# Optimization experiments

Hardware: AMD Instinct MI355X
Metric: run time of the kernel (lower is better)

The kernel has to match this reference:

```python
import jax, jax.numpy as jnp
import numpy as np

SEQ, WORD, EMBED, NHEAD = 2048, 1024, 128, 16


def setup_inputs() -> dict:
    key = jax.random.key(0)
    ks = jax.random.split(key, 6)
    sw = 1.0 / np.sqrt(WORD)  # xavier-ish scale for linear weights
    sp = 1.0 / np.sqrt(EMBED * NHEAD)
    return {
        "x": jax.random.normal(ks[0], (SEQ, WORD), jnp.float32),
        "Wq": jax.random.normal(ks[1], (NHEAD, WORD, EMBED), jnp.float32) * sw,
        "bq": jnp.zeros((NHEAD, EMBED), jnp.float32),
        "Wk": jax.random.normal(ks[2], (NHEAD, WORD, EMBED), jnp.float32) * sw,
        "bk": jnp.zeros((NHEAD, EMBED), jnp.float32),
        "Wv": jax.random.normal(ks[3], (NHEAD, WORD, EMBED), jnp.float32) * sw,
        "bv": jnp.zeros((NHEAD, EMBED), jnp.float32),
        "proj": jax.random.normal(ks[4], (NHEAD * EMBED, EMBED), jnp.float32) * sp,
    }


def reference(x, Wq, bq, Wk, bk, Wv, bv, proj):
    # Batched-head equivalent of the per-head Attention ModuleList loop.
    # x: [S, W]; Wq/Wk/Wv: [H, W, E]; b*: [H, E]; proj: [H*E, E]
    Q = jnp.einsum("sw,hwe->hse", x, Wq) + bq[:, None, :]
    K = jnp.einsum("sw,hwe->hse", x, Wk) + bk[:, None, :]
    V = jnp.einsum("sw,hwe->hse", x, Wv) + bv[:, None, :]
    scale = 1.0 / jnp.sqrt(jnp.asarray(EMBED, x.dtype))
    scores = jnp.einsum("hqe,hke->hqk", Q, K) * scale  # [H, S, S]
    attn = jax.nn.softmax(scores, axis=-1)
    Z = jnp.einsum("hqk,hke->hqe", attn, V)  # [H, S, E]
    # torch.cat([...], dim=1): per-head outputs side-by-side -> [S, H*E]
    Z_s = jnp.transpose(Z, (1, 0, 2)).reshape(x.shape[0], -1)
    return Z_s @ proj  # [S, E]
```

## Files before the change

kernel.cpp:

```cpp
#include <hip/hip_runtime.h>
#include <stdint.h>

#define GAS __attribute__((address_space(1)))
#define LAS __attribute__((address_space(3)))

typedef unsigned short u16;
typedef __attribute__((ext_vector_type(8))) __bf16 bf16x8;
typedef __attribute__((ext_vector_type(4))) float f32x4;
typedef __attribute__((ext_vector_type(4))) unsigned short u16x4;

#define SEQ 2048
#define WORD 1024
#define EMBED 128
#define NHEAD 16

__device__ __forceinline__ u16 f2b(float f) {
  return __builtin_bit_cast(u16, (__bf16)f);
}

__device__ __forceinline__ long qfrag_off(int qrow, int e) {
  return ((((long)(qrow >> 4)) * 4 + (e >> 5)) * 64 + ((e >> 3) & 3) * 16 +
          (qrow & 15)) * 8 + (e & 7);
}

__global__ __launch_bounds__(256) void cast_x_kernel(const float* __restrict__ x,
                                                     u16* __restrict__ xb) {
  int i = (blockIdx.x * 256 + threadIdx.x) * 4;
  float4 v = *(const float4*)(x + i);
  ushort4 o;
  o.x = f2b(v.x); o.y = f2b(v.y); o.z = f2b(v.z); o.w = f2b(v.w);
  *(ushort4*)(xb + i) = o;
}

__global__ __launch_bounds__(256) void transpose_cast_kernel(
    const float* __restrict__ s0, const float* __restrict__ s1,
    const float* __restrict__ s2, u16* __restrict__ d0, u16* __restrict__ d1,
    u16* __restrict__ d2, int R, int C, long stride, int zsel) {
  __shared__ float tile[32][33];
  const float* s;
  u16* d;
  if (zsel) {
    int z = blockIdx.z;
    int wsel = z >> 4, hh = z & 15;
    s = (wsel == 0 ? s0 : wsel == 1 ? s1 : s2) + (long)hh * stride;
    d = (wsel == 0 ? d0 : wsel == 1 ? d1 : d2) + (long)hh * stride;
  } else {
    s = s0; d = d0;
  }
  int r0 = blockIdx.x * 32, c0 = blockIdx.y * 32;
  int tx = threadIdx.x & 31, ty = threadIdx.x >> 5;
#pragma unroll
  for (int i = 0; i < 4; ++i)
    tile[ty + i * 8][tx] = s[(long)(r0 + ty + i * 8) * C + c0 + tx];
  __syncthreads();
#pragma unroll
  for (int i = 0; i < 4; ++i)
    d[(long)(c0 + ty + i * 8) * R + r0 + tx] = f2b(tile[tx][ty + i * 8]);
}

template <int MODE>
__device__ __forceinline__ void gemm128(const u16* __restrict__ A, const u16* __restrict__ B,
                                        void* __restrict__ Cp, int lda, int ldb, int ldc,
                                        int ksteps, const float* biasN, const float* biasM,
                                        float scale, int rowbase) {
  __shared__ u16 lA[128 * 64];
  __shared__ u16 lB[128 * 64];
  const int tid = threadIdx.x;
  const int l = tid & 63, w = tid >> 6;
  const int quad = l >> 4, ln = l & 15;
  const int wm = w >> 1, wn = w & 1;
  f32x4 acc[4][4] = {};
  for (int ks = 0; ks < ksteps; ++ks) {
    const u16* Ak = A + ks * 64;
    const u16* Bk = B + ks * 64;
    __syncthreads();
#pragma unroll
    for (int i = 0; i < 4; ++i) {
      int idx = w * 256 + i * 64 + l;
      int r = idx >> 3, cp = idx & 7;
      int cg = cp ^ (r & 7);
      __builtin_amdgcn_global_load_lds((const GAS void*)(Ak + (long)r * lda + cg * 8),
                                       (LAS void*)(lA + (w * 256 + i * 64) * 8), 16, 0, 0);
      __builtin_amdgcn_global_load_lds((const GAS void*)(Bk + (long)r * ldb + cg * 8),
                                       (LAS void*)(lB + (w * 256 + i * 64) * 8), 16, 0, 0);
    }
    __syncthreads();
    bf16x8 af[2][4], bfv[2][4];
#pragma unroll
    for (int kc = 0; kc < 2; ++kc) {
#pragma unroll
      for (int i = 0; i < 4; ++i) {
        int c = kc * 4 + quad;
        int rm = wm * 64 + i * 16 + ln;
        af[kc][i] = *(const bf16x8*)(lA + rm * 64 + ((c ^ (rm & 7)) * 8));
        int rn = wn * 64 + i * 16 + ln;
        bfv[kc][i] = *(const bf16x8*)(lB + rn * 64 + ((c ^ (rn & 7)) * 8));
      }
    }
#pragma unroll
    for (int kc = 0; kc < 2; ++kc)
#pragma unroll
      for (int i = 0; i < 4; ++i)
#pragma unroll
        for (int j = 0; j < 4; ++j)
          acc[i][j] = __builtin_amdgcn_mfma_f32_16x16x32_bf16(af[kc][i], bfv[kc][j],
                                                              acc[i][j], 0, 0, 0);
  }
#pragma unroll
  for (int i = 0; i < 4; ++i) {
#pragma unroll
    for (int j = 0; j < 4; ++j) {
      int row0 = wm * 64 + i * 16 + quad * 4;
      int col = wn * 64 + j * 16 + ln;
      float bn = biasN ? biasN[col] : 0.f;
#pragma unroll
      for (int reg = 0; reg < 4; ++reg) {
        int row = row0 + reg;
        float bm = biasM ? biasM[row] : 0.f;
        float v = (acc[i][j][reg] + bn + bm) * scale;
        if constexpr (MODE == 0) {
          ((float*)Cp)[(long)row * ldc + col] = v;
        } else if constexpr (MODE == 1) {
          ((u16*)Cp)[(long)row * ldc + col] = f2b(v);
        } else {
          ((u16*)Cp)[qfrag_off(rowbase + row, col)] = f2b(v);
        }
      }
    }
  }
}

__global__ __launch_bounds__(256, 3) void qkv_gemm_kernel(
    const u16* __restrict__ xb, const u16* __restrict__ Wqt, const u16* __restrict__ Wkt,
    const u16* __restrict__ Wvt, const float* __restrict__ bq, const float* __restrict__ bk,
    const float* __restrict__ bv, u16* __restrict__ Qf, u16* __restrict__ Km,
    u16* __restrict__ Vt) {
  const int t = blockIdx.x;
  const int h = blockIdx.y;
  const int which = blockIdx.z;
  const float qscale = 0.12753042123789493f;
  if (which == 0) {
    gemm128<2>(xb + t * 128 * WORD, Wqt + h * EMBED * WORD,
               Qf + (long)h * 262144, WORD, WORD, 0,
               WORD / 64, bq + h * EMBED, nullptr, qscale, t * 128);
  } else if (which == 1) {
    gemm128<1>(xb + t * 128 * WORD, Wkt + h * EMBED * WORD,
               Km + (long)h * SEQ * EMBED + t * 128 * EMBED, WORD, WORD, EMBED,
               WORD / 64, bk + h * EMBED, nullptr, 1.f, 0);
  } else {
    gemm128<1>(Wvt + h * EMBED * WORD, xb + t * 128 * WORD,
               Vt + (long)h * EMBED * SEQ + t * 128, WORD, WORD, SEQ,
               WORD / 64, nullptr, bv + h * EMBED, 1.f, 0);
  }
}

__global__ __launch_bounds__(256, 2) void attn_kernel(const u16* __restrict__ Qf,
                                                      const u16* __restrict__ Km,
                                                      const u16* __restrict__ Vt,
                                                      u16* __restrict__ Zs) {
  __shared__ u16 lKV[2][2][8192];
  __shared__ u16 lP[4][32 * 40];
  const int h = blockIdx.y, qb = blockIdx.x;
  const int tid = threadIdx.x;
  const int l = tid & 63, w = tid >> 6, quad = l >> 4, ln = l & 15;
  const int wr = w >> 1, wk = w & 1;
  const u16* Kh = Km + (long)h * SEQ * EMBED;
  const u16* Vh = Vt + (long)h * EMBED * SEQ;
  const u16* Qfh = Qf + (long)h * 262144;
  u16* Pw = lP[w];

  bf16x8 qf[2][4];
#pragma unroll
  for (int rs = 0; rs < 2; ++rs)
#pragma unroll
    for (int kc = 0; kc < 4; ++kc)
      qf[rs][kc] = *(const bf16x8*)(Qfh + (((qb * 4 + wr * 2 + rs) * 4 + kc) * 64 + l) * 8);

  const __bf16 ov = (ln == 0) ? (__bf16)1.0f : (__bf16)0.0f;
  const bf16x8 onesf = {ov, ov, ov, ov, ov, ov, ov, ov};

  f32x4 oacc[2][8] = {};
  f32x4 lacc[2] = {};

  auto stage = [&](int sup, int buf) {
#pragma unroll
    for (int j = 0; j < 4; ++j) {
      int ck = j * 256 + w * 64 + l;
      int kr = ck >> 4, cg = (ck & 15) ^ (kr & 15);
      __builtin_amdgcn_global_load_lds(
          (const GAS void*)(Kh + (sup * 64 + kr) * EMBED + cg * 8),
          (LAS void*)(&lKV[buf][0][(j * 256 + w * 64) * 8]), 16, 0, 0);
      int cv = j * 256 + w * 64 + l;
      int rv = cv >> 3, cgv = (cv & 7) ^ (rv & 7);
      __builtin_amdgcn_global_load_lds(
          (const GAS void*)(Vh + (long)rv * SEQ + sup * 64 + cgv * 8),
          (LAS void*)(&lKV[buf][1][(j * 256 + w * 64) * 8]), 16, 0, 0);
    }
  };

  stage(0, 0);
  for (int sup = 0; sup < SEQ / 64; ++sup) {
    const int cur = sup & 1;
    __syncthreads();
    if (sup + 1 < SEQ / 64) stage(sup + 1, cur ^ 1);
    const u16* Kb = lKV[cur][0];
    const u16* Vb = lKV[cur][1];
#pragma unroll
    for (int ns = 0; ns < 2; ++ns) {
      f32x4 sacc[2] = {};
#pragma unroll
      for (int kc = 0; kc < 4; ++kc) {
        int ks = wk * 32 + ns * 16 + ln;
        bf16x8 kf = *(const bf16x8*)(Kb + ks * 128 + (((kc * 4 + quad) ^ (ks & 15)) * 8));
#pragma unroll
        for (int rs = 0; rs < 2; ++rs)
          sacc[rs] = __builtin_amdgcn_mfma_f32_16x16x32_bf16(kf, qf[rs][kc],
                                                             sacc[rs], 0, 0, 0);
      }
#pragma unroll
      for (int rs = 0; rs < 2; ++rs) {
        u16x4 pk;
        pk.x = f2b(exp2f(sacc[rs][0]));
        pk.y = f2b(exp2f(sacc[rs][1]));
        pk.z = f2b(exp2f(sacc[rs][2]));
        pk.w = f2b(exp2f(sacc[rs][3]));
        *(u16x4*)(Pw + (rs * 16 + ln) * 40 + (ns * 4 + quad) * 4) = pk;
      }
    }
    bf16x8 pa[2];
#pragma unroll
    for (int rs = 0; rs < 2; ++rs)
      pa[rs] = *(const bf16x8*)(Pw + (rs * 16 + ln) * 40 + quad * 8);
    bf16x8 vf[8];
#pragma unroll
    for (int es = 0; es < 8; ++es) {
      int er = es * 16 + ln;
      vf[es] = *(const bf16x8*)(Vb + er * 64 + (((wk * 4 + quad) ^ (er & 7)) * 8));
    }
#pragma unroll
    for (int es = 0; es < 8; ++es)
#pragma unroll
      for (int rs = 0; rs < 2; ++rs)
        oacc[rs][es] = __builtin_amdgcn_mfma_f32_16x16x32_bf16(pa[rs], vf[es],
                                                               oacc[rs][es], 0, 0, 0);
#pragma unroll
    for (int rs = 0; rs < 2; ++rs)
      lacc[rs] = __builtin_amdgcn_mfma_f32_16x16x32_bf16(pa[rs], onesf, lacc[rs], 0, 0, 0);
  }
  __syncthreads();
  float* lO = (float*)lKV;
  float* lL = lO + 64 * 132;
  if (wk == 1) {
#pragma unroll
    for (int rs = 0; rs < 2; ++rs) {
#pragma unroll
      for (int es = 0; es < 8; ++es)
#pragma unroll
        for (int r = 0; r < 4; ++r)
          lO[(wr * 32 + rs * 16 + quad * 4 + r) * 132 + es * 16 + ln] = oacc[rs][es][r];
      if (ln == 0)
#pragma unroll
        for (int r = 0; r < 4; ++r)
          lL[wr * 32 + rs * 16 + quad * 4 + r] = lacc[rs][r];
    }
  }
  __syncthreads();
  if (wk == 0) {
#pragma unroll
    for (int rs = 0; rs < 2; ++rs)
#pragma unroll
      for (int r = 0; r < 4; ++r) {
        int grow = wr * 32 + rs * 16 + quad * 4 + r;
        float lsum = __shfl(lacc[rs][r], l & 48) + lL[grow];
        float rl = 1.f / lsum;
        int srow = qb * 64 + grow;
#pragma unroll
        for (int es = 0; es < 8; ++es) {
          float o = oacc[rs][es][r] + lO[grow * 132 + es * 16 + ln];
          Zs[(long)srow * (NHEAD * EMBED) + h * EMBED + es * 16 + ln] = f2b(o * rl);
        }
      }
  }
}

__global__ __launch_bounds__(256, 2) void final_gemm_kernel(const u16* __restrict__ Zs,
                                                            const u16* __restrict__ projT,
                                                            float* __restrict__ pbuf) {
  const int t = blockIdx.x;
  const int kc = blockIdx.y;
  gemm128<0>(Zs + (long)t * 128 * (NHEAD * EMBED) + kc * 256, projT + kc * 256,
             pbuf + (long)kc * SEQ * EMBED + t * 128 * EMBED,
             NHEAD * EMBED, NHEAD * EMBED, EMBED, 4, nullptr, nullptr, 1.f, 0);
}

__global__ __launch_bounds__(256) void reduce_kernel(const float* __restrict__ pbuf,
                                                     float* __restrict__ out) {
  int i = (blockIdx.x * 256 + threadIdx.x) * 4;
  float4 s = {0.f, 0.f, 0.f, 0.f};
#pragma unroll
  for (int kc = 0; kc < 8; ++kc) {
    float4 v = *(const float4*)(pbuf + (long)kc * SEQ * EMBED + i);
    s.x += v.x; s.y += v.y; s.z += v.z; s.w += v.w;
  }
  *(float4*)(out + i) = s;
}

extern "C" void kernel_launch(void* const* d_in, const int* in_sizes, int n_in,
                              void* d_out, int out_size, void* d_ws, size_t ws_size,
                              hipStream_t stream) {
  const float* x    = (const float*)d_in[0];
  const float* Wq   = (const float*)d_in[1];
  const float* bq   = (const float*)d_in[2];
  const float* Wk   = (const float*)d_in[3];
  const float* bk   = (const float*)d_in[4];
  const float* Wv   = (const float*)d_in[5];
  const float* bv   = (const float*)d_in[6];
  const float* proj = (const float*)d_in[7];
  float* out = (float*)d_out;

  char* ws = (char*)d_ws;
  u16* xb    = (u16*)(ws);
  u16* Wqt   = (u16*)(ws + (4L << 20));
  u16* Wkt   = (u16*)(ws + (8L << 20));
  u16* Wvt   = (u16*)(ws + (12L << 20));
  u16* projT = (u16*)(ws + (16L << 20));
  u16* Qf    = (u16*)(ws + (17L << 20));
  u16* Km    = (u16*)(ws + (26L << 20));
  u16* Vt    = (u16*)(ws + (35L << 20));
  u16* Zs    = (u16*)(ws + (44L << 20));
  float* pbuf = (float*)(ws);

  cast_x_kernel<<<dim3(SEQ * WORD / 1024), dim3(256), 0, stream>>>(x, xb);
  transpose_cast_kernel<<<dim3(WORD / 32, EMBED / 32, 48), dim3(256), 0, stream>>>(
      Wq, Wk, Wv, Wqt, Wkt, Wvt, WORD, EMBED, (long)WORD * EMBED, 1);
  transpose_cast_kernel<<<dim3(SEQ / 32, EMBED / 32, 1), dim3(256), 0, stream>>>(
      proj, nullptr, nullptr, projT, nullptr, nullptr, SEQ, EMBED, 0, 0);

  qkv_gemm_kernel<<<dim3(16, NHEAD, 3), dim3(256), 0, stream>>>(
      xb, Wqt, Wkt, Wvt, bq, bk, bv, Qf, Km, Vt);

  attn_kernel<<<dim3(32, NHEAD), dim3(256), 0, stream>>>(Qf, Km, Vt, Zs);

  final_gemm_kernel<<<dim3(16, 8), dim3(256), 0, stream>>>(Zs, projT, pbuf);
  reduce_kernel<<<dim3(SEQ * EMBED / 1024), dim3(256), 0, stream>>>(pbuf, out);
}
```

Measured before the change: 208.1 us.

## Store K and V in MFMA fragment layout and load directly to registers

The QKV GEMM now writes K and V in pre-swizzled MFMA fragment order, the same way Q already was. The attention kernel then loads K/V fragments straight from global memory into registers with software prefetch, instead of staging them through double-buffered LDS with barriers. It also linearises the grid so that consecutive blocks share a query block across heads. This removes the LDS staging and the per-iteration __syncthreads. The cost is that each wave re-reads K/V from global/L2 without sharing them through LDS, and register pressure rises.

```diff
diff --git a/kernel.cpp b/kernel.cpp
--- a/kernel.cpp
+++ b/kernel.cpp
@@ -18,9 +18,13 @@
   return __builtin_bit_cast(u16, (__bf16)f);
 }
 
-__device__ __forceinline__ long qfrag_off(int qrow, int e) {
-  return ((((long)(qrow >> 4)) * 4 + (e >> 5)) * 64 + ((e >> 3) & 3) * 16 +
-          (qrow & 15)) * 8 + (e & 7);
+__device__ __forceinline__ long qfrag_off(int row, int e) {
+  return ((((long)(row >> 4)) * 4 + (e >> 5)) * 64 + ((e >> 3) & 3) * 16 +
+          (row & 15)) * 8 + (e & 7);
+}
+__device__ __forceinline__ long vfrag_off(int er, int key) {
+  return (((((long)(key >> 5)) * 8) + (er >> 4)) * 64 +
+          ((key >> 3) & 3) * 16 + (er & 15)) * 8 + (key & 7);
 }
 
 __global__ __launch_bounds__(256) void cast_x_kernel(const float* __restrict__ x,
@@ -62,7 +66,7 @@
 __device__ __forceinline__ void gemm128(const u16* __restrict__ A, const u16* __restrict__ B,
                                         void* __restrict__ Cp, int lda, int ldb, int ldc,
                                         int ksteps, const float* biasN, const float* biasM,
-                                        float scale, int rowbase) {
+                                        float scale, int rowbase, int colbase) {
   __shared__ u16 lA[128 * 64];
   __shared__ u16 lB[128 * 64];
   const int tid = threadIdx.x;
@@ -122,8 +126,10 @@
           ((float*)Cp)[(long)row * ldc + col] = v;
         } else if constexpr (MODE == 1) {
           ((u16*)Cp)[(long)row * ldc + col] = f2b(v);
+        } else if constexpr (MODE == 2) {
+          ((u16*)Cp)[qfrag_off(rowbase + row, colbase + col)] = f2b(v);
         } else {
-          ((u16*)Cp)[qfrag_off(rowbase + row, col)] = f2b(v);
+          ((u16*)Cp)[vfrag_off(rowbase + row, colbase + col)] = f2b(v);
         }
       }
     }
@@ -133,8 +139,8 @@
 __global__ __launch_bounds__(256, 3) void qkv_gemm_kernel(
     const u16* __restrict__ xb, const u16* __restrict__ Wqt, const u16* __restrict__ Wkt,
     const u16* __restrict__ Wvt, const float* __restrict__ bq, const float* __restrict__ bk,
-    const float* __restrict__ bv, u16* __restrict__ Qf, u16* __restrict__ Km,
-    u16* __restrict__ Vt) {
+    const float* __restrict__ bv, u16* __restrict__ Qf, u16* __restrict__ Kf,
+    u16* __restrict__ Vf) {
   const int t = blockIdx.x;
   const int h = blockIdx.y;
   const int which = blockIdx.z;
@@ -142,32 +148,30 @@
   if (which == 0) {
     gemm128<2>(xb + t * 128 * WORD, Wqt + h * EMBED * WORD,
                Qf + (long)h * 262144, WORD, WORD, 0,
-               WORD / 64, bq + h * EMBED, nullptr, qscale, t * 128);
+               WORD / 64, bq + h * EMBED, nullptr, qscale, t * 128, 0);
   } else if (which == 1) {
-    gemm128<1>(xb + t * 128 * WORD, Wkt + h * EMBED * WORD,
-               Km + (long)h * SEQ * EMBED + t * 128 * EMBED, WORD, WORD, EMBED,
-               WORD / 64, bk + h * EMBED, nullptr, 1.f, 0);
+    gemm128<2>(xb + t * 128 * WORD, Wkt + h * EMBED * WORD,
+               Kf + (long)h * 262144, WORD, WORD, 0,
+               WORD / 64, bk + h * EMBED, nullptr, 1.f, t * 128, 0);
   } else {
-    gemm128<1>(Wvt + h * EMBED * WORD, xb + t * 128 * WORD,
-               Vt + (long)h * EMBED * SEQ + t * 128, WORD, WORD, SEQ,
-               WORD / 64, nullptr, bv + h * EMBED, 1.f, 0);
+    gemm128<3>(Wvt + h * EMBED * WORD, xb + t * 128 * WORD,
+               Vf + (long)h * 262144, WORD, WORD, 0,
+               WORD / 64, nullptr, bv + h * EMBED, 1.f, 0, t * 128);
   }
 }
 
 __global__ __launch_bounds__(256, 2) void attn_kernel(const u16* __restrict__ Qf,
-                                                      const u16* __restrict__ Km,
-                                                      const u16* __restrict__ Vt,
+                                                      const u16* __restrict__ Kf,
+                                                      const u16* __restrict__ Vf,
                                                       u16* __restrict__ Zs) {
-  __shared__ u16 lKV[2][2][8192];
-  __shared__ u16 lP[4][32 * 40];
-  const int h = blockIdx.y, qb = blockIdx.x;
+  __shared__ char smem[34304];
+  const int bid = blockIdx.x;
+  const int h = bid & 15, qb = bid >> 4;
   const int tid = threadIdx.x;
   const int l = tid & 63, w = tid >> 6, quad = l >> 4, ln = l & 15;
   const int wr = w >> 1, wk = w & 1;
-  const u16* Kh = Km + (long)h * SEQ * EMBED;
-  const u16* Vh = Vt + (long)h * EMBED * SEQ;
   const u16* Qfh = Qf + (long)h * 262144;
-  u16* Pw = lP[w];
+  u16* Pw = (u16*)smem + w * 1280;
 
   bf16x8 qf[2][4];
 #pragma unroll
@@ -182,73 +186,62 @@
   f32x4 oacc[2][8] = {};
   f32x4 lacc[2] = {};
 
-  auto stage = [&](int sup, int buf) {
-#pragma unroll
-    for (int j = 0; j < 4; ++j) {
-      int ck = j * 256 + w * 64 + l;
-      int kr = ck >> 4, cg = (ck & 15) ^ (kr & 15);
-      __builtin_amdgcn_global_load_lds(
-          (const GAS void*)(Kh + (sup * 64 + kr) * EMBED + cg * 8),
-          (LAS void*)(&lKV[buf][0][(j * 256 + w * 64) * 8]), 16, 0, 0);
-      int cv = j * 256 + w * 64 + l;
-      int rv = cv >> 3, cgv = (cv & 7) ^ (rv & 7);
-      __builtin_amdgcn_global_load_lds(
-          (const GAS void*)(Vh + (long)rv * SEQ + sup * 64 + cgv * 8),
-          (LAS void*)(&lKV[buf][1][(j * 256 + w * 64) * 8]), 16, 0, 0);
-    }
-  };
-
-  stage(0, 0);
-  for (int sup = 0; sup < SEQ / 64; ++sup) {
-    const int cur = sup & 1;
-    __syncthreads();
-    if (sup + 1 < SEQ / 64) stage(sup + 1, cur ^ 1);
-    const u16* Kb = lKV[cur][0];
-    const u16* Vb = lKV[cur][1];
-#pragma unroll
-    for (int ns = 0; ns < 2; ++ns) {
-      f32x4 sacc[2] = {};
+  const u16* kp = Kf + (long)h * 262144 + wk * 131072 + l * 8;
+  const u16* vp = Vf + (long)h * 262144 + wk * 131072 + l * 8;
+
+  bf16x8 kf[8], vf[8];
+#pragma unroll
+  for (int t = 0; t < 8; ++t) kf[t] = *(const bf16x8*)(kp + t * 512);
+#pragma unroll
+  for (int es = 0; es < 8; ++es) vf[es] = *(const bf16x8*)(vp + es * 512);
+
+  for (int i = 0; i < 32; ++i) {
+    f32x4 sacc[2][2] = {};
+#pragma unroll
+    for (int ns = 0; ns < 2; ++ns)
 #pragma unroll
       for (int kc = 0; kc < 4; ++kc) {
-        int ks = wk * 32 + ns * 16 + ln;
-        bf16x8 kf = *(const bf16x8*)(Kb + ks * 128 + (((kc * 4 + quad) ^ (ks & 15)) * 8));
+        bf16x8 k8 = kf[ns * 4 + kc];
 #pragma unroll
         for (int rs = 0; rs < 2; ++rs)
-          sacc[rs] = __builtin_amdgcn_mfma_f32_16x16x32_bf16(kf, qf[rs][kc],
-                                                             sacc[rs], 0, 0, 0);
-      }
-#pragma unroll
-      for (int rs = 0; rs < 2; ++rs) {
+          sacc[rs][ns] = __builtin_amdgcn_mfma_f32_16x16x32_bf16(k8, qf[rs][kc],
+                                                                 sacc[rs][ns], 0, 0, 0);
+      }
+    kp += 4096;
+#pragma unroll
+    for (int t = 0; t < 8; ++t) kf[t] = *(const bf16x8*)(kp + t * 512);
+#pragma unroll
+    for (int rs = 0; rs < 2; ++rs)
+#pragma unroll
+      for (int ns = 0; ns < 2; ++ns) {
         u16x4 pk;
-        pk.x = f2b(exp2f(sacc[rs][0]));
-        pk.y = f2b(exp2f(sacc[rs][1]));
-        pk.z = f2b(exp2f(sacc[rs][2]));
-        pk.w = f2b(exp2f(sacc[rs][3]));
+        pk.x = f2b(exp2f(sacc[rs][ns][0]));
+        pk.y = f2b(exp2f(sacc[rs][ns][1]));
+        pk.z = f2b(exp2f(sacc[rs][ns][2]));
+        pk.w = f2b(exp2f(sacc[rs][ns][3]));
         *(u16x4*)(Pw + (rs * 16 + ln) * 40 + (ns * 4 + quad) * 4) = pk;
       }
-    }
     bf16x8 pa[2];
 #pragma unroll
     for (int rs = 0; rs < 2; ++rs)
       pa[rs] = *(const bf16x8*)(Pw + (rs * 16 + ln) * 40 + quad * 8);
-    bf16x8 vf[8];
 #pragma unroll
     for (int es = 0; es < 8; ++es) {
-      int er = es * 16 + ln;
-      vf[es] = *(const bf16x8*)(Vb + er * 64 + (((wk * 4 + quad) ^ (er & 7)) * 8));
-    }
-#pragma unroll
-    for (int es = 0; es < 8; ++es)
+      bf16x8 v8 = vf[es];
 #pragma unroll
       for (int rs = 0; rs < 2; ++rs)
-        oacc[rs][es] = __builtin_amdgcn_mfma_f32_16x16x32_bf16(pa[rs], vf[es],
+        oacc[rs][es] = __builtin_amdgcn_mfma_f32_16x16x32_bf16(pa[rs], v8,
                                                                oacc[rs][es], 0, 0, 0);
+    }
 #pragma unroll
     for (int rs = 0; rs < 2; ++rs)
       lacc[rs] = __builtin_amdgcn_mfma_f32_16x16x32_bf16(pa[rs], onesf, lacc[rs], 0, 0, 0);
+    vp += 4096;
+#pragma unroll
+    for (int es = 0; es < 8; ++es) vf[es] = *(const bf16x8*)(vp + es * 512);
   }
   __syncthreads();
-  float* lO = (float*)lKV;
+  float* lO = (float*)smem;
   float* lL = lO + 64 * 132;
   if (wk == 1) {
 #pragma unroll
@@ -290,7 +283,7 @@
   const int kc = blockIdx.y;
   gemm128<0>(Zs + (long)t * 128 * (NHEAD * EMBED) + kc * 256, projT + kc * 256,
              pbuf + (long)kc * SEQ * EMBED + t * 128 * EMBED,
-             NHEAD * EMBED, NHEAD * EMBED, EMBED, 4, nullptr, nullptr, 1.f, 0);
+             NHEAD * EMBED, NHEAD * EMBED, EMBED, 4, nullptr, nullptr, 1.f, 0, 0);
 }
 
 __global__ __launch_bounds__(256) void reduce_kernel(const float* __restrict__ pbuf,
@@ -325,8 +318,8 @@
   u16* Wvt   = (u16*)(ws + (12L << 20));
   u16* projT = (u16*)(ws + (16L << 20));
   u16* Qf    = (u16*)(ws + (17L << 20));
-  u16* Km    = (u16*)(ws + (26L << 20));
-  u16* Vt    = (u16*)(ws + (35L << 20));
+  u16* Kf    = (u16*)(ws + (26L << 20));
+  u16* Vf    = (u16*)(ws + (35L << 20));
   u16* Zs    = (u16*)(ws + (44L << 20));
   float* pbuf = (float*)(ws);
 
@@ -337,9 +330,9 @@
       proj, nullptr, nullptr, projT, nullptr, nullptr, SEQ, EMBED, 0, 0);
 
   qkv_gemm_kernel<<<dim3(16, NHEAD, 3), dim3(256), 0, stream>>>(
-      xb, Wqt, Wkt, Wvt, bq, bk, bv, Qf, Km, Vt);
-
-  attn_kernel<<<dim3(32, NHEAD), dim3(256), 0, stream>>>(Qf, Km, Vt, Zs);
+      xb, Wqt, Wkt, Wvt, bq, bk, bv, Qf, Kf, Vf);
+
+  attn_kernel<<<dim3(512), dim3(256), 0, stream>>>(Qf, Kf, Vf, Zs);
 
   final_gemm_kernel<<<dim3(16, 8), dim3(256), 0, stream>>>(Zs, projT, pbuf);
   reduce_kernel<<<dim3(SEQ * EMBED / 1024), dim3(256), 0, stream>>>(pbuf, out);
```

Measured after the change: 210.3 us. No clear change (+1.1%).
